# Kernel tuning notes

Measured on AMD Instinct MI355X. Metric: run time of the kernel, lower is better.

Reference implementation:

```python
import jax, jax.numpy as jnp
import numpy as np

HEADS = 16
PHI = (1.0 + np.sqrt(5.0)) / 2.0


def setup_inputs() -> dict:
    key = jax.random.key(0)
    k1, k2, k3, k4 = jax.random.split(key, 4)
    B, L, D = 2, 2048, 1024
    x = jax.random.normal(k1, (B, L, D), dtype=jnp.float32)
    # nn.Linear(dim, 3*dim, bias=False): store as [D, 3D] for x @ W
    w_qkv = jax.random.normal(k2, (D, 3 * D), dtype=jnp.float32) * (D ** -0.5)
    w_proj = jax.random.normal(k3, (D, D), dtype=jnp.float32) * (D ** -0.5)
    b_proj = jax.random.normal(k4, (D,), dtype=jnp.float32) * 0.01
    return {"x": x, "w_qkv": w_qkv, "w_proj": w_proj, "b_proj": b_proj}


def phi_bias(L):
    # pos[i] = (i * phi) mod 1 ; bias = log(exp(-|pos_i - pos_j|) + 1e-8)
    pos = (jnp.arange(L, dtype=jnp.float32) * PHI) % 1.0
    dist = jnp.abs(pos[:, None] - pos[None, :])  # [L, L]
    return jnp.log(jnp.exp(-dist) + 1e-8)


def reference(x, w_qkv, w_proj, b_proj):
    B, L, D = x.shape
    H = HEADS
    Dh = D // H
    scale = Dh ** -0.5
    qkv = (x @ w_qkv).reshape(B, L, 3, H, Dh)
    q = jnp.transpose(qkv[:, :, 0], (0, 2, 1, 3))  # [B, H, L, Dh]
    k = jnp.transpose(qkv[:, :, 1], (0, 2, 1, 3))
    v = jnp.transpose(qkv[:, :, 2], (0, 2, 1, 3))
    attn = jnp.einsum("bhid,bhjd->bhij", q, k) * scale  # [B, H, L, L]
    attn = attn + phi_bias(L)[None, None]  # additive phi-distance bias
    attn = jax.nn.softmax(attn, axis=-1)
    out = jnp.einsum("bhij,bhjd->bhid", attn, v)  # [B, H, L, Dh]
    out = jnp.transpose(out, (0, 2, 1, 3)).reshape(B, L, D)
    return out @ w_proj + b_proj
```

## Files before the change

kernel.cpp:

```cpp
#include <hip/hip_runtime.h>
#include <math.h>


typedef _Float16 f16;
typedef _Float16 f16x4 __attribute__((ext_vector_type(4)));
typedef _Float16 f16x8 __attribute__((ext_vector_type(8)));
typedef float f32x4 __attribute__((ext_vector_type(4)));

#define MFMA32(a, b, c) __builtin_amdgcn_mfma_f32_16x16x32_f16(a, b, c, 0, 0, 0)

static constexpr int Bsz = 2, Lseq = 2048, Dm = 1024, H = 16, Dh = 64;
static constexpr int Mtot = Bsz * Lseq;
static constexpr int NQKV = 3 * Dm;
static constexpr float PHI_F = 1.61803398874989484820f;
static constexpr float LOG2E = 1.44269504088896f;
static constexpr float QS = 0.125f * LOG2E;
static constexpr float CSTEP = 0.55417527999932633f;

__device__ __forceinline__ void load16_to_lds(const f16* g, f16* l) {
  __builtin_amdgcn_global_load_lds(
      (const __attribute__((address_space(1))) unsigned int*)g,
      (__attribute__((address_space(3))) unsigned int*)l, 16, 0, 0);
}

__global__ __launch_bounds__(256) void cast_f32_f16(const float* __restrict__ in,
                                                    f16* __restrict__ out, int n) {
  int i = (blockIdx.x * 256 + threadIdx.x) * 4;
  if (i < n) {
    float4 v = *reinterpret_cast<const float4*>(in + i);
    f16 t[4] = {(f16)v.x, (f16)v.y, (f16)v.z, (f16)v.w};
    *reinterpret_cast<uint2*>(out + i) = *reinterpret_cast<uint2*>(t);
  }
}

__global__ __launch_bounds__(256) void transpose_cast(const float* __restrict__ in,
                                                      f16* __restrict__ out,
                                                      int K, int N) {
  __shared__ float tile[32][33];
  int n0 = blockIdx.x * 32, k0 = blockIdx.y * 32;
  int tx = threadIdx.x & 31, ty = threadIdx.x >> 5;
#pragma unroll
  for (int r = 0; r < 32; r += 8)
    tile[ty + r][tx] = in[(size_t)(k0 + ty + r) * N + n0 + tx];
  __syncthreads();
#pragma unroll
  for (int r = 0; r < 32; r += 8)
    out[(size_t)(n0 + ty + r) * K + k0 + tx] = (f16)tile[tx][ty + r];
}

__global__ __launch_bounds__(256) void v_transpose(const f16* __restrict__ in,
                                                   f16* __restrict__ out) {
  __shared__ f16 td[64][68];
  int bh = blockIdx.y, l0 = blockIdx.x * 64;
  int tid = threadIdx.x;
  const f16* src = in + (size_t)bh * Lseq * Dh;
#pragma unroll
  for (int c = tid; c < 512; c += 256) {
    int row = c >> 3, col = (c & 7) * 8;
    uint4 v = *reinterpret_cast<const uint4*>(src + (size_t)(l0 + row) * Dh + col);
    f16 tmp[8];
    *reinterpret_cast<uint4*>(tmp) = v;
#pragma unroll
    for (int j = 0; j < 8; j++) td[col + j][row] = tmp[j];
  }
  __syncthreads();
  f16* dst = out + (size_t)bh * Dh * Lseq;
#pragma unroll
  for (int c = tid; c < 512; c += 256) {
    int d = c >> 3, co = c & 7;
    int jh = co >> 2, qd = co & 3;
    f16 tmp[8];
#pragma unroll
    for (int e = 0; e < 4; e++) tmp[e] = td[d][jh * 32 + qd * 4 + e];
#pragma unroll
    for (int e = 0; e < 4; e++) tmp[4 + e] = td[d][jh * 32 + 16 + qd * 4 + e];
    *reinterpret_cast<uint4*>(dst + (size_t)d * Lseq + l0 + co * 8) =
        *reinterpret_cast<uint4*>(tmp);
  }
}

template <int MODE>
__global__ __launch_bounds__(256) void gemm_f16(
    const f16* __restrict__ A, const f16* __restrict__ Bt,
    int M, int N, int K,
    f16* __restrict__ qb, f16* __restrict__ kb, f16* __restrict__ vl,
    float* __restrict__ out, const float* __restrict__ bias) {
  constexpr int BM = (MODE == 0) ? 128 : 64;
  constexpr int MI = BM / 32;
  constexpr int AI = BM / 32;
  __shared__ f16 As[BM * 64];
  __shared__ f16 Bs[128 * 64];

  int tid = threadIdx.x;
  int wave = tid >> 6, lane = tid & 63;
  int quad = lane >> 4, l16 = lane & 15;
  int wm = (wave >> 1) * (MI * 16), wn = (wave & 1) * 64;

  int lid = blockIdx.x;
  int xcd = lid & 7, t = lid >> 3;
  int m0, n0;
  if (MODE == 0) {
    int mg = xcd >> 1, ng = xcd & 1;
    m0 = (mg * 8 + t / 12) * 128;
    n0 = (ng * 12 + t % 12) * 128;
  } else {
    m0 = (xcd * 8 + (t >> 3)) * 64;
    n0 = (t & 7) * 128;
  }

  const int gu = (lane & 7) ^ (lane >> 3);
  const f16* gA[AI];
  f16* lA[AI];
#pragma unroll
  for (int i = 0; i < AI; i++) {
    int it = wave * AI + i;
    gA[i] = A + (size_t)(m0 + it * 8 + (lane >> 3)) * K + gu * 8;
    lA[i] = As + it * 512;
  }
  const f16* gB[4];
  f16* lB[4];
#pragma unroll
  for (int i = 0; i < 4; i++) {
    int it = wave * 4 + i;
    gB[i] = Bt + (size_t)(n0 + it * 8 + (lane >> 3)) * K + gu * 8;
    lB[i] = Bs + it * 512;
  }

  f32x4 acc[MI][4] = {};

  for (int k0 = 0; k0 < K; k0 += 64) {
#pragma unroll
    for (int i = 0; i < AI; i++) load16_to_lds(gA[i] + k0, lA[i]);
#pragma unroll
    for (int i = 0; i < 4; i++) load16_to_lds(gB[i] + k0, lB[i]);
    __syncthreads();
#pragma unroll
    for (int s = 0; s < 2; s++) {
      f16x8 a[MI], b[4];
#pragma unroll
      for (int i = 0; i < MI; i++) {
        int row = wm + i * 16 + l16;
        a[i] = *reinterpret_cast<const f16x8*>(
            As + row * 64 + (((s * 4 + quad) ^ (l16 & 7)) * 8));
      }
#pragma unroll
      for (int j = 0; j < 4; j++) {
        int row = wn + j * 16 + l16;
        b[j] = *reinterpret_cast<const f16x8*>(
            Bs + row * 64 + (((s * 4 + quad) ^ (l16 & 7)) * 8));
      }
#pragma unroll
      for (int i = 0; i < MI; i++)
#pragma unroll
        for (int j = 0; j < 4; j++)
          acc[i][j] = MFMA32(a[i], b[j], acc[i][j]);
    }
    __syncthreads();
  }

#pragma unroll
  for (int i = 0; i < MI; i++) {
#pragma unroll
    for (int j = 0; j < 4; j++) {
      int n = n0 + wn + j * 16 + l16;
#pragma unroll
      for (int r = 0; r < 4; r++) {
        int m = m0 + wm + i * 16 + quad * 4 + r;
        if (MODE == 0) {
          int ty = n >> 10;
          int df = n & 1023;
          int h = df >> 6, dh = df & 63;
          int b = m >> 11, l = m & 2047;
          size_t idx = (((size_t)(b * H + h)) * Lseq + l) * Dh + dh;
          if (ty == 0)
            qb[idx] = (f16)(acc[i][j][r] * QS);
          else if (ty == 1)
            kb[idx] = (f16)acc[i][j][r];
          else
            vl[idx] = (f16)acc[i][j][r];
        } else {
          out[(size_t)m * N + n] = acc[i][j][r] + bias[n];
        }
      }
    }
  }
}

__global__ __launch_bounds__(256, 4) void attn_kernel(
    const f16* __restrict__ qb,
    const f16* __restrict__ kb,
    const f16* __restrict__ vb,
    f16* __restrict__ ctx) {
  __shared__ __align__(16) unsigned char smem[16640];
  f16* Ks = (f16*)smem;
  f16* Vs = (f16*)(smem + 8192);

  int bh = blockIdx.y;
  int q0 = blockIdx.x * 64;
  int tid = threadIdx.x, wave = tid >> 6, lane = tid & 63;
  int quad = lane >> 4, l16 = lane & 15;
  int jhalf = wave >> 1, qhalf = wave & 1;

  f16x8 qfrag[2][2];
  float pq[2];
#pragma unroll
  for (int set = 0; set < 2; set++) {
    int q = q0 + qhalf * 32 + set * 16 + l16;
    const f16* Qrow = qb + ((size_t)bh * Lseq + q) * Dh;
    qfrag[set][0] = *reinterpret_cast<const f16x8*>(Qrow + quad * 8);
    qfrag[set][1] = *reinterpret_cast<const f16x8*>(Qrow + 32 + quad * 8);
    pq[set] = fmodf((float)q * PHI_F, 1.0f);
  }

  float pk[2][4];
#pragma unroll
  for (int jb = 0; jb < 2; jb++)
#pragma unroll
    for (int r = 0; r < 4; r++) {
      int j = jhalf * 32 + jb * 16 + quad * 4 + r;
      pk[jb][r] = fmodf((float)j * PHI_F, 1.0f);
    }

  const f16* Kbh = kb + (size_t)bh * Lseq * Dh;
  const f16* Vbh = vb + (size_t)bh * Dh * Lseq;
  const int gu = (lane & 7) ^ (lane >> 3);
  const f16* gK[2];
  const f16* gV[2];
  f16* lK[2];
  f16* lV[2];
#pragma unroll
  for (int i = 0; i < 2; i++) {
    int g8 = (wave * 2 + i) * 8 + (lane >> 3);
    gK[i] = Kbh + (size_t)g8 * Dh + gu * 8;
    gV[i] = Vbh + (size_t)g8 * Lseq + gu * 8;
    lK[i] = Ks + (wave * 2 + i) * 512;
    lV[i] = Vs + (wave * 2 + i) * 512;
  }

  const f16 one = (f16)1.0f;
  const f16x8 ones8 = {one, one, one, one, one, one, one, one};

  f32x4 acc_o[2][4] = {};
  f32x4 acc_l[2] = {};

  for (int j0 = 0; j0 < Lseq; j0 += 64) {
    __syncthreads();
#pragma unroll
    for (int i = 0; i < 2; i++) {
      load16_to_lds(gK[i] + (size_t)j0 * Dh, lK[i]);
      load16_to_lds(gV[i] + j0, lV[i]);
    }
    __syncthreads();

    f32x4 accs[2][2] = {};
#pragma unroll
    for (int s = 0; s < 2; s++)
#pragma unroll
      for (int jb = 0; jb < 2; jb++) {
        f16x8 kf = *reinterpret_cast<const f16x8*>(
            Ks + (jhalf * 32 + jb * 16 + l16) * 64 + (((s * 4 + quad) ^ (l16 & 7)) * 8));
        accs[0][jb] = MFMA32(kf, qfrag[0][s], accs[0][jb]);
        accs[1][jb] = MFMA32(kf, qfrag[1][s], accs[1][jb]);
      }

    f16x8 pf8[2];
#pragma unroll
    for (int set = 0; set < 2; set++) {
#pragma unroll
      for (int jb = 0; jb < 2; jb++) {
        float p[4];
#pragma unroll
        for (int r = 0; r < 4; r++) {
          float d = pq[set] - pk[jb][r];
          float arg = fmaf(-LOG2E, fabsf(d), accs[set][jb][r]);
          p[r] = __builtin_amdgcn_exp2f(arg);
        }
        auto lo = __builtin_amdgcn_cvt_pkrtz(p[0], p[1]);
        auto hi = __builtin_amdgcn_cvt_pkrtz(p[2], p[3]);
        pf8[set][jb * 4 + 0] = lo[0];
        pf8[set][jb * 4 + 1] = lo[1];
        pf8[set][jb * 4 + 2] = hi[0];
        pf8[set][jb * 4 + 3] = hi[1];
      }
      acc_l[set] = MFMA32(ones8, pf8[set], acc_l[set]);
    }
#pragma unroll
    for (int jb = 0; jb < 2; jb++)
#pragma unroll
      for (int r = 0; r < 4; r++)
        pk[jb][r] = __builtin_amdgcn_fractf(pk[jb][r] + CSTEP);

#pragma unroll
    for (int dblk = 0; dblk < 4; dblk++) {
      int row = dblk * 16 + l16;
      f16x8 va = *reinterpret_cast<const f16x8*>(
          Vs + row * 64 + (((jhalf * 4 + quad) ^ (l16 & 7)) * 8));
      acc_o[0][dblk] = MFMA32(va, pf8[0], acc_o[0][dblk]);
      acc_o[1][dblk] = MFMA32(va, pf8[1], acc_o[1][dblk]);
    }
  }

  __syncthreads();
  float* Oex = (float*)smem;
  float* Lex = (float*)(smem + 16384);
  if (jhalf == 1) {
#pragma unroll
    for (int set = 0; set < 2; set++) {
#pragma unroll
      for (int dblk = 0; dblk < 4; dblk++)
#pragma unroll
        for (int r = 0; r < 4; r++)
          Oex[(((qhalf * 2 + set) * 4 + dblk) * 16 + quad * 4 + r) * 16 + l16] =
              acc_o[set][dblk][r];
      if (quad == 0) Lex[(qhalf * 2 + set) * 16 + l16] = acc_l[set][0];
    }
  }
  __syncthreads();
  if (jhalf == 0) {
    int b = bh >> 4, h = bh & 15;
#pragma unroll
    for (int set = 0; set < 2; set++) {
      float ltot = acc_l[set][0] + Lex[(qhalf * 2 + set) * 16 + l16];
      float inv = 1.0f / ltot;
      int q = q0 + qhalf * 32 + set * 16 + l16;
      f16* crow = ctx + (size_t)(b * Lseq + q) * Dm + h * 64;
#pragma unroll
      for (int dblk = 0; dblk < 4; dblk++) {
        f16x4 o;
#pragma unroll
        for (int r = 0; r < 4; r++) {
          float full = acc_o[set][dblk][r] +
              Oex[(((qhalf * 2 + set) * 4 + dblk) * 16 + quad * 4 + r) * 16 + l16];
          o[r] = (f16)(full * inv);
        }
        *reinterpret_cast<uint2*>(crow + dblk * 16 + quad * 4) =
            *reinterpret_cast<uint2*>(&o);
      }
    }
  }
}

extern "C" void kernel_launch(void* const* d_in, const int* in_sizes, int n_in,
                              void* d_out, int out_size, void* d_ws, size_t ws_size,
                              hipStream_t stream) {
  const float* x      = (const float*)d_in[0];
  const float* w_qkv  = (const float*)d_in[1];
  const float* w_proj = (const float*)d_in[2];
  const float* b_proj = (const float*)d_in[3];
  float* out = (float*)d_out;

  f16* xb    = (f16*)d_ws;
  f16* wqkvT = xb + (size_t)Mtot * Dm;
  f16* wpT   = wqkvT + (size_t)NQKV * Dm;
  f16* qb    = wpT + (size_t)Dm * Dm;
  f16* kb    = qb + (size_t)Bsz * H * Lseq * Dh;
  f16* vb    = kb + (size_t)Bsz * H * Lseq * Dh;
  f16* ctx   = vb + (size_t)Bsz * H * Lseq * Dh;
  f16* vl    = ctx;

  cast_f32_f16<<<(Mtot * Dm) / (256 * 4), 256, 0, stream>>>(x, xb, Mtot * Dm);
  transpose_cast<<<dim3(NQKV / 32, Dm / 32), 256, 0, stream>>>(w_qkv, wqkvT, Dm, NQKV);
  transpose_cast<<<dim3(Dm / 32, Dm / 32), 256, 0, stream>>>(w_proj, wpT, Dm, Dm);

  gemm_f16<0><<<768, 256, 0, stream>>>(
      xb, wqkvT, Mtot, NQKV, Dm, qb, kb, vl, nullptr, nullptr);

  v_transpose<<<dim3(Lseq / 64, Bsz * H), 256, 0, stream>>>(vl, vb);

  attn_kernel<<<dim3(Lseq / 64, Bsz * H), 256, 0, stream>>>(qb, kb, vb, ctx);

  gemm_f16<1><<<512, 256, 0, stream>>>(
      ctx, wpT, Mtot, Dm, Dm, nullptr, nullptr, nullptr, out, b_proj);
}
```

Baseline: 194.8 us.

## Fuse V transpose into QKV GEMM epilogue with tiled V layout

Removes the separate v_transpose kernel by having the QKV GEMM epilogue write V directly in a blocked transposed layout (64-key tiles of Dh x 64, permuted to match the attention kernel's fragment order), using 8-byte vector stores. The attention kernel's V load addressing is changed to read contiguous 4096-element tiles per key block. This saves one kernel launch and a full read/write pass over V, at the cost of a more complex epilogue address computation.

```diff
diff --git a/kernel.cpp b/kernel.cpp
--- a/kernel.cpp
+++ b/kernel.cpp
@@ -48,42 +48,11 @@
     out[(size_t)(n0 + ty + r) * K + k0 + tx] = (f16)tile[tx][ty + r];
 }
 
-__global__ __launch_bounds__(256) void v_transpose(const f16* __restrict__ in,
-                                                   f16* __restrict__ out) {
-  __shared__ f16 td[64][68];
-  int bh = blockIdx.y, l0 = blockIdx.x * 64;
-  int tid = threadIdx.x;
-  const f16* src = in + (size_t)bh * Lseq * Dh;
-#pragma unroll
-  for (int c = tid; c < 512; c += 256) {
-    int row = c >> 3, col = (c & 7) * 8;
-    uint4 v = *reinterpret_cast<const uint4*>(src + (size_t)(l0 + row) * Dh + col);
-    f16 tmp[8];
-    *reinterpret_cast<uint4*>(tmp) = v;
-#pragma unroll
-    for (int j = 0; j < 8; j++) td[col + j][row] = tmp[j];
-  }
-  __syncthreads();
-  f16* dst = out + (size_t)bh * Dh * Lseq;
-#pragma unroll
-  for (int c = tid; c < 512; c += 256) {
-    int d = c >> 3, co = c & 7;
-    int jh = co >> 2, qd = co & 3;
-    f16 tmp[8];
-#pragma unroll
-    for (int e = 0; e < 4; e++) tmp[e] = td[d][jh * 32 + qd * 4 + e];
-#pragma unroll
-    for (int e = 0; e < 4; e++) tmp[4 + e] = td[d][jh * 32 + 16 + qd * 4 + e];
-    *reinterpret_cast<uint4*>(dst + (size_t)d * Lseq + l0 + co * 8) =
-        *reinterpret_cast<uint4*>(tmp);
-  }
-}
-
 template <int MODE>
 __global__ __launch_bounds__(256) void gemm_f16(
     const f16* __restrict__ A, const f16* __restrict__ Bt,
     int M, int N, int K,
-    f16* __restrict__ qb, f16* __restrict__ kb, f16* __restrict__ vl,
+    f16* __restrict__ qb, f16* __restrict__ kb, f16* __restrict__ vb,
     float* __restrict__ out, const float* __restrict__ bias) {
   constexpr int BM = (MODE == 0) ? 128 : 64;
   constexpr int MI = BM / 32;
@@ -163,22 +132,40 @@
 #pragma unroll
     for (int j = 0; j < 4; j++) {
       int n = n0 + wn + j * 16 + l16;
-#pragma unroll
-      for (int r = 0; r < 4; r++) {
-        int m = m0 + wm + i * 16 + quad * 4 + r;
-        if (MODE == 0) {
-          int ty = n >> 10;
-          int df = n & 1023;
-          int h = df >> 6, dh = df & 63;
-          int b = m >> 11, l = m & 2047;
-          size_t idx = (((size_t)(b * H + h)) * Lseq + l) * Dh + dh;
-          if (ty == 0)
-            qb[idx] = (f16)(acc[i][j][r] * QS);
-          else if (ty == 1)
-            kb[idx] = (f16)acc[i][j][r];
-          else
-            vl[idx] = (f16)acc[i][j][r];
+      if (MODE == 0) {
+        int ty = n >> 10;
+        int df = n & 1023;
+        int h = df >> 6, dh = df & 63;
+        int mb = m0 + wm + i * 16 + quad * 4;
+        int b = mb >> 11, l = mb & 2047;
+        int bhh = b * H + h;
+        if (ty == 2) {
+          int jj = l & 63;
+          int jh = jj >> 5, rem = jj & 31;
+          int qd = (rem & 15) >> 2;
+          int e0 = (rem >= 16) ? 4 : 0;
+          f16x4 tmp;
+#pragma unroll
+          for (int r = 0; r < 4; r++) tmp[r] = (f16)acc[i][j][r];
+          *reinterpret_cast<uint2*>(
+              vb + (size_t)bhh * (Dh * Lseq) + (l >> 6) * 4096 + dh * 64 +
+              (jh * 4 + qd) * 8 + e0) = *reinterpret_cast<uint2*>(&tmp);
         } else {
+          size_t idx = (((size_t)bhh) * Lseq + l) * Dh + dh;
+          if (ty == 0) {
+#pragma unroll
+            for (int r = 0; r < 4; r++)
+              qb[idx + (size_t)r * Dh] = (f16)(acc[i][j][r] * QS);
+          } else {
+#pragma unroll
+            for (int r = 0; r < 4; r++)
+              kb[idx + (size_t)r * Dh] = (f16)acc[i][j][r];
+          }
+        }
+      } else {
+#pragma unroll
+        for (int r = 0; r < 4; r++) {
+          int m = m0 + wm + i * 16 + quad * 4 + r;
           out[(size_t)m * N + n] = acc[i][j][r] + bias[n];
         }
       }
@@ -232,7 +219,7 @@
   for (int i = 0; i < 2; i++) {
     int g8 = (wave * 2 + i) * 8 + (lane >> 3);
     gK[i] = Kbh + (size_t)g8 * Dh + gu * 8;
-    gV[i] = Vbh + (size_t)g8 * Lseq + gu * 8;
+    gV[i] = Vbh + (size_t)g8 * 64 + gu * 8;
     lK[i] = Ks + (wave * 2 + i) * 512;
     lV[i] = Vs + (wave * 2 + i) * 512;
   }
@@ -248,7 +235,7 @@
 #pragma unroll
     for (int i = 0; i < 2; i++) {
       load16_to_lds(gK[i] + (size_t)j0 * Dh, lK[i]);
-      load16_to_lds(gV[i] + j0, lV[i]);
+      load16_to_lds(gV[i] + (size_t)j0 * 64, lV[i]);
     }
     __syncthreads();
 
@@ -356,16 +343,13 @@
   f16* kb    = qb + (size_t)Bsz * H * Lseq * Dh;
   f16* vb    = kb + (size_t)Bsz * H * Lseq * Dh;
   f16* ctx   = vb + (size_t)Bsz * H * Lseq * Dh;
-  f16* vl    = ctx;
 
   cast_f32_f16<<<(Mtot * Dm) / (256 * 4), 256, 0, stream>>>(x, xb, Mtot * Dm);
   transpose_cast<<<dim3(NQKV / 32, Dm / 32), 256, 0, stream>>>(w_qkv, wqkvT, Dm, NQKV);
   transpose_cast<<<dim3(Dm / 32, Dm / 32), 256, 0, stream>>>(w_proj, wpT, Dm, Dm);
 
   gemm_f16<0><<<768, 256, 0, stream>>>(
-      xb, wqkvT, Mtot, NQKV, Dm, qb, kb, vl, nullptr, nullptr);
-
-  v_transpose<<<dim3(Lseq / 64, Bsz * H), 256, 0, stream>>>(vl, vb);
+      xb, wqkvT, Mtot, NQKV, Dm, qb, kb, vb, nullptr, nullptr);
 
   attn_kernel<<<dim3(Lseq / 64, Bsz * H), 256, 0, stream>>>(qb, kb, vb, ctx);
 
```

Result: faster. 189.7 us (-2.6%).
